# Optimization experiments

Hardware: AMD Instinct MI355X
Metric: run time of the kernel (lower is better)

The kernel has to match this reference:

```python
import jax, jax.numpy as jnp
import numpy as np

N_NODES = 50000
N_EDGES = 1600000
IN_C, HID_C, OUT_C = 1433, 128, 47


def setup_inputs() -> dict:
    key = jax.random.key(0)
    ks = jax.random.split(key, 5)
    x = jax.random.normal(ks[0], (N_NODES, IN_C), dtype=jnp.float32)
    edge_index = jax.random.randint(ks[1], (2, N_EDGES), 0, N_NODES, dtype=jnp.int32)
    # Glorot-ish init scaled by fan-in
    W1 = jax.random.normal(ks[2], (IN_C, HID_C), dtype=jnp.float32) / np.sqrt(IN_C)
    W2 = jax.random.normal(ks[3], (HID_C, HID_C), dtype=jnp.float32) / np.sqrt(HID_C)
    W3 = jax.random.normal(ks[4], (HID_C, OUT_C), dtype=jnp.float32) / np.sqrt(HID_C)
    b1 = jnp.zeros((HID_C,), jnp.float32)
    b2 = jnp.zeros((HID_C,), jnp.float32)
    b3 = jnp.zeros((OUT_C,), jnp.float32)
    return {"x": x, "edge_index": edge_index, "W1": W1, "b1": b1,
            "W2": W2, "b2": b2, "W3": W3, "b3": b3}


def _gcn_norm(edge_index, n_nodes, dtype):
    # PyG GCNConv default: add self-loops, symmetric D^-1/2 A D^-1/2 norm.
    loops = jnp.arange(n_nodes, dtype=edge_index.dtype)
    src = jnp.concatenate([edge_index[0], loops])
    dst = jnp.concatenate([edge_index[1], loops])
    deg = jax.ops.segment_sum(jnp.ones(src.shape[0], dtype), dst, num_segments=n_nodes)
    dinv = jax.lax.rsqrt(jnp.maximum(deg, 1.0))  # deg >= 1 due to self-loops
    norm = dinv[src] * dinv[dst]  # [E + N]
    return src, dst, norm


def _gcn_layer(h, W, b, src, dst, norm, n_nodes):
    hw = h @ W                       # [N, C_out] dense transform first (cheaper)
    msg = hw[src] * norm[:, None]    # gather + per-edge scale
    out = jax.ops.segment_sum(msg, dst, num_segments=n_nodes)  # scatter-add
    return out + b


def reference(x, edge_index, W1, b1, W2, b2, W3, b3):
    n = x.shape[0]
    src, dst, norm = _gcn_norm(edge_index, n, x.dtype)
    h = jax.nn.relu(_gcn_layer(x, W1, b1, src, dst, norm, n))
    # dropout is identity in eval mode (training=False)
    h = jax.nn.relu(_gcn_layer(h, W2, b2, src, dst, norm, n))
    return _gcn_layer(h, W3, b3, src, dst, norm, n)
```

## Files before the change

### kernel.cpp

```cpp
#include <hip/hip_runtime.h>
#include <math.h>
#include <stdint.h>

#define N_NODES 50000
#define N_EDGES 1600000
#define IN_C    1433
#define HID_C   128
#define OUT_C   47
#define KPAD1   1440

typedef unsigned short u16;

__device__ inline u16 f2bf(float x, float& hf) {
    unsigned u = __float_as_uint(x);
    unsigned r = (u + 0x7FFFu + ((u >> 16) & 1u)) & 0xFFFF0000u;
    hf = __uint_as_float(r);
    return (u16)(r >> 16);
}

__device__ inline void gld_lds16(const void* g, const void* lds) {
    __builtin_amdgcn_global_load_lds(
        (const __attribute__((address_space(1))) unsigned int*)(unsigned long long)(uintptr_t)g,
        (__attribute__((address_space(3))) unsigned int*)(unsigned long long)(unsigned)(uintptr_t)lds,
        16, 0, 0);
}

__device__ inline void wg_barrier() {
    asm volatile("" ::: "memory");
    __builtin_amdgcn_s_barrier();
    asm volatile("" ::: "memory");
}

__global__ __launch_bounds__(256) void k_zero_i(int* p, int n) {
    int i = blockIdx.x * 256 + threadIdx.x;
    if (i < n) p[i] = 0;
}

__global__ __launch_bounds__(256) void k_count(const int* __restrict__ dst, int* __restrict__ cnt) {
    int e = blockIdx.x * 256 + threadIdx.x;
    if (e < N_EDGES) atomicAdd(&cnt[dst[e]], 1);
}

__global__ __launch_bounds__(256) void k_dinv(const int* __restrict__ cnt, float* __restrict__ dinv) {
    int i = blockIdx.x * 256 + threadIdx.x;
    if (i < N_NODES) dinv[i] = rsqrtf(1.0f + (float)cnt[i]);
}

__global__ __launch_bounds__(1024) void k_scan(const int* __restrict__ cnt, int* __restrict__ row_start) {
    __shared__ int sums[1024];
    const int t = threadIdx.x;
    const int CH = (N_NODES + 1023) / 1024;
    const int base = t * CH;
    int s = 0;
    for (int j = 0; j < CH; ++j) { int idx = base + j; if (idx < N_NODES) s += cnt[idx]; }
    sums[t] = s;
    __syncthreads();
    for (int off = 1; off < 1024; off <<= 1) {
        int v = (t >= off) ? sums[t - off] : 0;
        __syncthreads();
        sums[t] += v;
        __syncthreads();
    }
    int run = (t == 0) ? 0 : sums[t - 1];
    for (int j = 0; j < CH; ++j) {
        int idx = base + j;
        if (idx < N_NODES) { row_start[idx] = run; run += cnt[idx]; }
    }
    if (t == 1023) row_start[N_NODES] = N_EDGES;
}

__global__ __launch_bounds__(256) void k_fill(
    const int* __restrict__ src, const int* __restrict__ dst,
    const int* __restrict__ row_start, int* __restrict__ cursor,
    int* __restrict__ csr_src)
{
    int e = blockIdx.x * 256 + threadIdx.x;
    if (e >= N_EDGES) return;
    int t = dst[e];
    int pos = row_start[t] + atomicAdd(&cursor[t], 1);
    csr_src[pos] = src[e];
}

__global__ __launch_bounds__(256) void k_wsplit(
    const float* __restrict__ W, int K, int Kpad,
    u16* __restrict__ Thi, u16* __restrict__ Tlo)
{
    int id = blockIdx.x * 256 + threadIdx.x;
    if (id >= 128 * Kpad) return;
    int n = id / Kpad, k = id - n * Kpad;
    float v = (k < K) ? W[(long)k * HID_C + n] : 0.f;
    float hf; u16 h = f2bf(v, hf);
    float d;  u16 l = f2bf(v - hf, d);
    Thi[id] = h; Tlo[id] = l;
}

template<bool RELU_A>
__global__ __launch_bounds__(256) void k_gemm_mfma(
    const float* __restrict__ A, const u16* __restrict__ BThi,
    const u16* __restrict__ BTlo, float* __restrict__ C,
    int M, int K, int Kpad, int lda)
{
    using bf16x8 = __attribute__((ext_vector_type(8))) short;
    using f32x4  = __attribute__((ext_vector_type(4))) float;

    __shared__ float Af[3][2048];
    __shared__ u16  Bhs[3][4096];
    __shared__ u16  Bls[3][4096];

    const int tid  = threadIdx.x;
    const int wave = tid >> 6, lane = tid & 63;
    const int lr   = lane & 15, quad = lane >> 4;
    const int wm   = (wave >> 1) * 32, wn = (wave & 1) * 64;
    const int m0   = blockIdx.x * 64;

    f32x4 acc[2][4];
#pragma unroll
    for (int i = 0; i < 2; ++i)
#pragma unroll
        for (int j = 0; j < 4; ++j)
#pragma unroll
            for (int r = 0; r < 4; ++r) acc[i][j][r] = 0.f;

    const int nk = (K + 31) >> 5;

    auto stageB = [&](int t, int buf) {
        const int k0 = t * 32;
#pragma unroll
        for (int i = 0; i < 2; ++i) {
            const int gc  = wave * 128 + i * 64;
            const int g   = gc + lane;
            const int row = g >> 2, c = g & 3;
            const int q   = c ^ ((row >> 1) & 3);
            const long goff = (long)row * Kpad + k0 + q * 8;
            gld_lds16(BThi + goff, &Bhs[buf][gc * 8]);
            gld_lds16(BTlo + goff, &Bls[buf][gc * 8]);
        }
    };
    auto stageA = [&](int t, int buf) {
        const int k0 = t * 32;
        if (k0 + 32 <= K) {
#pragma unroll
            for (int i = 0; i < 2; ++i) {
                const int gc  = wave * 128 + i * 64;
                const int g   = gc + lane;
                const int row = g >> 3, c = g & 7;
                const int q   = c ^ (row & 7);
                int gm = m0 + row; if (gm >= M) gm = M - 1;
                gld_lds16(A + (long)gm * lda + k0 + q * 4, &Af[buf][gc * 4]);
            }
        } else {
#pragma unroll
            for (int i = 0; i < 2; ++i) {
                const int g   = wave * 128 + i * 64 + lane;
                const int row = g >> 3, c = g & 7;
                const int q   = c ^ (row & 7);
                int gm = m0 + row; if (gm >= M) gm = M - 1;
                const float* p = A + (long)gm * lda;
                const int kb = k0 + q * 4;
                float4 v;
                v.x = (kb + 0 < K) ? p[kb + 0] : 0.f;
                v.y = (kb + 1 < K) ? p[kb + 1] : 0.f;
                v.z = (kb + 2 < K) ? p[kb + 2] : 0.f;
                v.w = (kb + 3 < K) ? p[kb + 3] : 0.f;
                *(float4*)&Af[buf][g * 4] = v;
            }
            asm volatile("s_waitcnt lgkmcnt(0)" ::: "memory");
        }
    };

    stageA(0, 0); stageB(0, 0);
    if (nk > 1) { stageA(1, 1); stageB(1, 1); }

    for (int t = 0; t < nk; ++t) {
        const int buf = t % 3;
        if (t + 2 < nk) {
            const int nb = (t + 2) % 3;
            stageA(t + 2, nb); stageB(t + 2, nb);
            asm volatile("s_waitcnt vmcnt(12)" ::: "memory");
        } else if (t + 1 < nk) {
            asm volatile("s_waitcnt vmcnt(6)" ::: "memory");
        } else {
            asm volatile("s_waitcnt vmcnt(0)" ::: "memory");
        }
        wg_barrier();

        bf16x8 ah[2], al[2];
#pragma unroll
        for (int i = 0; i < 2; ++i) {
            const int row = wm + i * 16 + lr;
            const int rx  = row & 7;
            f32x4 x0 = *(const f32x4*)&Af[buf][row * 32 + (((2 * quad)     ^ rx) * 4)];
            f32x4 x1 = *(const f32x4*)&Af[buf][row * 32 + (((2 * quad + 1) ^ rx) * 4)];
            float a8[8] = {x0[0], x0[1], x0[2], x0[3], x1[0], x1[1], x1[2], x1[3]};
#pragma unroll
            for (int c = 0; c < 8; ++c) {
                float x = RELU_A ? fmaxf(a8[c], 0.f) : a8[c];
                float hf; u16 h = f2bf(x, hf);
                float d;  u16 l = f2bf(x - hf, d);
                ah[i][c] = (short)h; al[i][c] = (short)l;
            }
        }
        bf16x8 bh[4], bl[4];
#pragma unroll
        for (int j = 0; j < 4; ++j) {
            const int row = wn + j * 16 + lr;
            const int cs  = quad ^ ((row >> 1) & 3);
            bh[j] = *(const bf16x8*)&Bhs[buf][row * 32 + cs * 8];
            bl[j] = *(const bf16x8*)&Bls[buf][row * 32 + cs * 8];
        }
#pragma unroll
        for (int i = 0; i < 2; ++i)
#pragma unroll
            for (int j = 0; j < 4; ++j) {
                acc[i][j] = __builtin_amdgcn_mfma_f32_16x16x32_bf16(ah[i], bh[j], acc[i][j], 0, 0, 0);
                acc[i][j] = __builtin_amdgcn_mfma_f32_16x16x32_bf16(ah[i], bl[j], acc[i][j], 0, 0, 0);
                acc[i][j] = __builtin_amdgcn_mfma_f32_16x16x32_bf16(al[i], bh[j], acc[i][j], 0, 0, 0);
            }
        wg_barrier();
    }

#pragma unroll
    for (int i = 0; i < 2; ++i)
#pragma unroll
        for (int r = 0; r < 4; ++r) {
            int row = m0 + wm + i * 16 + quad * 4 + r;
            if (row < M) {
#pragma unroll
                for (int j = 0; j < 4; ++j)
                    C[(long)row * HID_C + wn + j * 16 + lr] = acc[i][j][r];
            }
        }
}

template<int BN, bool RELU_A, bool BIAS>
__global__ __launch_bounds__(256) void k_gemm(
    const float* __restrict__ A, const float* __restrict__ B,
    const float* __restrict__ bias, float* __restrict__ C,
    int M, int N, int K, int lda, int ldb, int ldc)
{
    constexpr int BM = 64, BK = 16;
    constexpr int TNV = BN / 64;
    __shared__ float As[BK][BM + 4];
    __shared__ float Bs[BK][BN];

    const int tid = threadIdx.x;
    const int tm = tid >> 4;
    const int tn = tid & 15;
    const int m0 = blockIdx.x * BM;
    const int n0 = blockIdx.y * BN;

    float acc[4][TNV * 4];
#pragma unroll
    for (int r = 0; r < 4; ++r)
#pragma unroll
        for (int c = 0; c < TNV * 4; ++c) acc[r][c] = 0.f;

    for (int k0 = 0; k0 < K; k0 += BK) {
        {
            int kk = tid & 15;
            int r0 = tid >> 4;
#pragma unroll
            for (int it = 0; it < 4; ++it) {
                int r = r0 + 16 * it;
                int gm = m0 + r, gk = k0 + kk;
                float v = 0.f;
                if (gm < M && gk < K) v = A[(long)gm * lda + gk];
                if (RELU_A) v = fmaxf(v, 0.f);
                As[kk][r] = v;
            }
        }
        {
            constexpr int KPP = 256 / BN;
            int n  = tid % BN;
            int kb = tid / BN;
#pragma unroll
            for (int it = 0; it < BK / KPP; ++it) {
                int kk = kb + KPP * it;
                int gk = k0 + kk, gn = n0 + n;
                float v = 0.f;
                if (gk < K && gn < N) v = B[(long)gk * ldb + gn];
                Bs[kk][n] = v;
            }
        }
        __syncthreads();
#pragma unroll
        for (int kk = 0; kk < BK; ++kk) {
            float4 a = *(const float4*)&As[kk][tm * 4];
            float av[4] = {a.x, a.y, a.z, a.w};
#pragma unroll
            for (int j = 0; j < TNV; ++j) {
                float4 b = *(const float4*)&Bs[kk][tn * 4 + 64 * j];
                float bv[4] = {b.x, b.y, b.z, b.w};
#pragma unroll
                for (int r = 0; r < 4; ++r)
#pragma unroll
                    for (int c = 0; c < 4; ++c)
                        acc[r][c + j * 4] += av[r] * bv[c];
            }
        }
        __syncthreads();
    }
#pragma unroll
    for (int r = 0; r < 4; ++r) {
        int gm = m0 + tm * 4 + r;
        if (gm >= M) continue;
#pragma unroll
        for (int j = 0; j < TNV; ++j)
#pragma unroll
            for (int c = 0; c < 4; ++c) {
                int gn = n0 + tn * 4 + 64 * j + c;
                if (gn < N) {
                    float v = acc[r][c + j * 4];
                    if (BIAS) v += bias[gn];
                    C[(long)gm * ldc + gn] = v;
                }
            }
    }
}

template<bool RELU_IN, bool BIAS>
__global__ __launch_bounds__(256) void k_aggregate(
    const float2* __restrict__ hw, const int* __restrict__ row_start,
    const int* __restrict__ csr_src, const float* __restrict__ dinv,
    const float* __restrict__ bias, float2* __restrict__ out)
{
    const int tid = threadIdx.x;
    const int node = blockIdx.x * 4 + (tid >> 6);
    if (node >= N_NODES) return;
    const int lane = tid & 63;

    float dt = dinv[node];
    float2 v = hw[(long)node * 64 + lane];
    if (RELU_IN) { v.x = fmaxf(v.x, 0.f); v.y = fmaxf(v.y, 0.f); }
    float2 acc = {0.f, 0.f};

    const int e1 = row_start[node + 1];
    int e = row_start[node];
    for (; e + 4 <= e1; e += 4) {
        int s0 = csr_src[e],     s1 = csr_src[e + 1];
        int s2 = csr_src[e + 2], s3 = csr_src[e + 3];
        float w0 = dinv[s0], w1 = dinv[s1], w2 = dinv[s2], w3 = dinv[s3];
        float2 u0 = hw[(long)s0 * 64 + lane];
        float2 u1 = hw[(long)s1 * 64 + lane];
        float2 u2 = hw[(long)s2 * 64 + lane];
        float2 u3 = hw[(long)s3 * 64 + lane];
        if (RELU_IN) {
            u0.x = fmaxf(u0.x, 0.f); u0.y = fmaxf(u0.y, 0.f);
            u1.x = fmaxf(u1.x, 0.f); u1.y = fmaxf(u1.y, 0.f);
            u2.x = fmaxf(u2.x, 0.f); u2.y = fmaxf(u2.y, 0.f);
            u3.x = fmaxf(u3.x, 0.f); u3.y = fmaxf(u3.y, 0.f);
        }
        acc.x += w0 * u0.x + w1 * u1.x + w2 * u2.x + w3 * u3.x;
        acc.y += w0 * u0.y + w1 * u1.y + w2 * u2.y + w3 * u3.y;
    }
    for (; e + 2 <= e1; e += 2) {
        int s0 = csr_src[e], s1 = csr_src[e + 1];
        float w0 = dinv[s0], w1 = dinv[s1];
        float2 u0 = hw[(long)s0 * 64 + lane];
        float2 u1 = hw[(long)s1 * 64 + lane];
        if (RELU_IN) {
            u0.x = fmaxf(u0.x, 0.f); u0.y = fmaxf(u0.y, 0.f);
            u1.x = fmaxf(u1.x, 0.f); u1.y = fmaxf(u1.y, 0.f);
        }
        acc.x += w0 * u0.x + w1 * u1.x;
        acc.y += w0 * u0.y + w1 * u1.y;
    }
    if (e < e1) {
        int s0 = csr_src[e];
        float w0 = dinv[s0];
        float2 u0 = hw[(long)s0 * 64 + lane];
        if (RELU_IN) { u0.x = fmaxf(u0.x, 0.f); u0.y = fmaxf(u0.y, 0.f); }
        acc.x += w0 * u0.x;
        acc.y += w0 * u0.y;
    }

    float2 r;
    r.x = dt * (acc.x + dt * v.x);
    r.y = dt * (acc.y + dt * v.y);
    if (BIAS) {
        float2 b = ((const float2*)bias)[lane];
        r.x += b.x; r.y += b.y;
    }
    out[(long)node * 64 + lane] = r;
}

__global__ __launch_bounds__(256) void k_aggregate47(
    const float* __restrict__ hw, const int* __restrict__ row_start,
    const int* __restrict__ csr_src, const float* __restrict__ dinv,
    const float* __restrict__ bias, float* __restrict__ out)
{
    const int tid = threadIdx.x;
    const int node = blockIdx.x * 4 + (tid >> 6);
    if (node >= N_NODES) return;
    const int lane = tid & 63;
    if (lane >= OUT_C) return;

    float dt = dinv[node];
    float v = hw[(long)node * 48 + lane];
    float acc = 0.f;

    const int e1 = row_start[node + 1];
    int e = row_start[node];
    for (; e + 4 <= e1; e += 4) {
        int s0 = csr_src[e],     s1 = csr_src[e + 1];
        int s2 = csr_src[e + 2], s3 = csr_src[e + 3];
        float w0 = dinv[s0], w1 = dinv[s1], w2 = dinv[s2], w3 = dinv[s3];
        float u0 = hw[(long)s0 * 48 + lane];
        float u1 = hw[(long)s1 * 48 + lane];
        float u2 = hw[(long)s2 * 48 + lane];
        float u3 = hw[(long)s3 * 48 + lane];
        acc += w0 * u0 + w1 * u1 + w2 * u2 + w3 * u3;
    }
    for (; e + 2 <= e1; e += 2) {
        int s0 = csr_src[e], s1 = csr_src[e + 1];
        float w0 = dinv[s0], w1 = dinv[s1];
        float u0 = hw[(long)s0 * 48 + lane];
        float u1 = hw[(long)s1 * 48 + lane];
        acc += w0 * u0 + w1 * u1;
    }
    if (e < e1) {
        int s0 = csr_src[e];
        acc += dinv[s0] * hw[(long)s0 * 48 + lane];
    }

    out[(long)node * OUT_C + lane] = dt * (acc + dt * v) + bias[lane];
}

extern "C" void kernel_launch(void* const* d_in, const int* in_sizes, int n_in,
                              void* d_out, int out_size, void* d_ws, size_t ws_size,
                              hipStream_t stream) {
    const float* x  = (const float*)d_in[0];
    const int*   ei = (const int*)  d_in[1];
    const float* W1 = (const float*)d_in[2];
    const float* b1 = (const float*)d_in[3];
    const float* W2 = (const float*)d_in[4];
    const float* b2 = (const float*)d_in[5];
    const float* W3 = (const float*)d_in[6];
    const float* b3 = (const float*)d_in[7];
    float* out = (float*)d_out;
    const int* src = ei;
    const int* dst = ei + N_EDGES;

    char* ws = (char*)d_ws;
    float* dinv      = (float*)(ws + 0);
    int*   cnt       = (int*)  (ws + 200192);
    int*   cursor    = (int*)  (ws + 400384);
    int*   row_start = (int*)  (ws + 600576);
    int*   csr_src   = (int*)  (ws + 801280);
    float* bufA      = (float*)(ws + 7201280);
    float* bufB      = (float*)(ws + 32801280);
    u16*   W1Thi     = (u16*)  (ws + 58401280);
    u16*   W1Tlo     = (u16*)  (ws + 58769920);
    u16*   W2Thi     = (u16*)  (ws + 59138560);
    u16*   W2Tlo     = (u16*)  (ws + 59171328);

    dim3 blk(256);
    const int gN  = (N_NODES + 255) / 256;
    const int gE  = (N_EDGES + 255) / 256;
    const int gAg = (N_NODES + 3) / 4;
    const int gMf = (N_NODES + 63) / 64;
    dim3 gGemm((N_NODES + 63) / 64, 1);

    k_zero_i<<<gN, blk, 0, stream>>>(cnt, N_NODES);
    k_zero_i<<<gN, blk, 0, stream>>>(cursor, N_NODES);
    k_count<<<gE, blk, 0, stream>>>(dst, cnt);
    k_dinv<<<gN, blk, 0, stream>>>(cnt, dinv);
    k_scan<<<1, 1024, 0, stream>>>(cnt, row_start);
    k_fill<<<gE, blk, 0, stream>>>(src, dst, row_start, cursor, csr_src);

    k_wsplit<<<(128 * KPAD1 + 255) / 256, blk, 0, stream>>>(W1, IN_C, KPAD1, W1Thi, W1Tlo);
    k_wsplit<<<(128 * HID_C + 255) / 256, blk, 0, stream>>>(W2, HID_C, HID_C, W2Thi, W2Tlo);

    k_gemm_mfma<false><<<gMf, blk, 0, stream>>>(x, W1Thi, W1Tlo, bufA, N_NODES, IN_C, KPAD1, IN_C);
    k_aggregate<false, true><<<gAg, blk, 0, stream>>>(
        (const float2*)bufA, row_start, csr_src, dinv, b1, (float2*)bufB);

    k_gemm_mfma<true><<<gMf, blk, 0, stream>>>(bufB, W2Thi, W2Tlo, bufA, N_NODES, HID_C, HID_C, HID_C);
    k_aggregate<false, true><<<gAg, blk, 0, stream>>>(
        (const float2*)bufA, row_start, csr_src, dinv, b2, (float2*)bufB);

    k_gemm<64, true, false><<<gGemm, blk, 0, stream>>>(
        bufB, W3, nullptr, bufA, N_NODES, OUT_C, HID_C, HID_C, OUT_C, 48);
    k_aggregate47<<<gAg, blk, 0, stream>>>(
        bufA, row_start, csr_src, dinv, b3, out);
}
```

Before: 696.7 us.

## Deepen A-tile prefetch to four stages and unroll aggregation gathers by eight

The GEMM now keeps four LDS buffers for the A tile and prefetches A three K-steps ahead, while B stays three-buffered and two steps ahead. The vmcnt wait counts are retuned for the new issue order. The sparse aggregation kernel gains an 8-way unrolled edge loop so more independent neighbor gathers are in flight. The extra A buffer adds 8KB of LDS, which may lower occupancy. The hand-tuned vmcnt values are a correctness risk if the per-stage load counts are not what they assume.

```diff
diff --git a/kernel.cpp b/kernel.cpp
--- a/kernel.cpp
+++ b/kernel.cpp
@@ -103,7 +103,7 @@
     using bf16x8 = __attribute__((ext_vector_type(8))) short;
     using f32x4  = __attribute__((ext_vector_type(4))) float;
 
-    __shared__ float Af[3][2048];
+    __shared__ float Af[4][2048];
     __shared__ u16  Bhs[3][4096];
     __shared__ u16  Bls[3][4096];
 
@@ -168,17 +168,23 @@
         }
     };
 
-    stageA(0, 0); stageB(0, 0);
-    if (nk > 1) { stageA(1, 1); stageB(1, 1); }
+    stageA(0, 0);
+    if (nk > 1) stageA(1, 1);
+    stageB(0, 0);
+    if (nk > 2) stageA(2, 2);
+    if (nk > 1) stageB(1, 1);
 
     for (int t = 0; t < nk; ++t) {
-        const int buf = t % 3;
-        if (t + 2 < nk) {
-            const int nb = (t + 2) % 3;
-            stageA(t + 2, nb); stageB(t + 2, nb);
+        const int ba = t & 3, bb = t % 3;
+        if (t + 3 < nk) {
+            stageA(t + 3, (t + 3) & 3);
+            stageB(t + 2, (t + 2) % 3);
             asm volatile("s_waitcnt vmcnt(12)" ::: "memory");
-        } else if (t + 1 < nk) {
-            asm volatile("s_waitcnt vmcnt(6)" ::: "memory");
+        } else if (t + 3 == nk) {
+            stageB(t + 2, (t + 2) % 3);
+            asm volatile("s_waitcnt vmcnt(10)" ::: "memory");
+        } else if (t + 2 == nk) {
+            asm volatile("s_waitcnt vmcnt(4)" ::: "memory");
         } else {
             asm volatile("s_waitcnt vmcnt(0)" ::: "memory");
         }
@@ -189,8 +195,8 @@
         for (int i = 0; i < 2; ++i) {
             const int row = wm + i * 16 + lr;
             const int rx  = row & 7;
-            f32x4 x0 = *(const f32x4*)&Af[buf][row * 32 + (((2 * quad)     ^ rx) * 4)];
-            f32x4 x1 = *(const f32x4*)&Af[buf][row * 32 + (((2 * quad + 1) ^ rx) * 4)];
+            f32x4 x0 = *(const f32x4*)&Af[ba][row * 32 + (((2 * quad)     ^ rx) * 4)];
+            f32x4 x1 = *(const f32x4*)&Af[ba][row * 32 + (((2 * quad + 1) ^ rx) * 4)];
             float a8[8] = {x0[0], x0[1], x0[2], x0[3], x1[0], x1[1], x1[2], x1[3]};
 #pragma unroll
             for (int c = 0; c < 8; ++c) {
@@ -205,8 +211,8 @@
         for (int j = 0; j < 4; ++j) {
             const int row = wn + j * 16 + lr;
             const int cs  = quad ^ ((row >> 1) & 3);
-            bh[j] = *(const bf16x8*)&Bhs[buf][row * 32 + cs * 8];
-            bl[j] = *(const bf16x8*)&Bls[buf][row * 32 + cs * 8];
+            bh[j] = *(const bf16x8*)&Bhs[bb][row * 32 + cs * 8];
+            bl[j] = *(const bf16x8*)&Bls[bb][row * 32 + cs * 8];
         }
 #pragma unroll
         for (int i = 0; i < 2; ++i)
@@ -336,6 +342,23 @@
 
     const int e1 = row_start[node + 1];
     int e = row_start[node];
+    for (; e + 8 <= e1; e += 8) {
+        int s[8];
+#pragma unroll
+        for (int q = 0; q < 8; ++q) s[q] = csr_src[e + q];
+        float w[8];
+#pragma unroll
+        for (int q = 0; q < 8; ++q) w[q] = dinv[s[q]];
+        float2 u[8];
+#pragma unroll
+        for (int q = 0; q < 8; ++q) u[q] = hw[(long)s[q] * 64 + lane];
+#pragma unroll
+        for (int q = 0; q < 8; ++q) {
+            if (RELU_IN) { u[q].x = fmaxf(u[q].x, 0.f); u[q].y = fmaxf(u[q].y, 0.f); }
+            acc.x += w[q] * u[q].x;
+            acc.y += w[q] * u[q].y;
+        }
+    }
     for (; e + 4 <= e1; e += 4) {
         int s0 = csr_src[e],     s1 = csr_src[e + 1];
         int s2 = csr_src[e + 2], s3 = csr_src[e + 3];
```

New measurement: 694.8 us. Within noise of the previous version (-0.3%).
